# Optimization experiments

Measured on AMD Instinct MI355X. Metric: run time of the kernel, lower is better.

Reference implementation:

```python
import jax, jax.numpy as jnp
import numpy as np

B, S, RNN, ATTH = 256, 196, 1024, 512  # batch, att_size, rnn_size, att_h_size


def setup_inputs() -> dict:
    key = jax.random.key(0)
    k1, k2, k3, k4, k5, k6, k7 = jax.random.split(key, 7)
    h = jax.random.normal(k1, (B, RNN), dtype=jnp.float32)
    att_feats = jax.random.normal(k2, (B, S, RNN), dtype=jnp.float32)
    p_att_feats = jax.random.normal(k3, (B, S, ATTH), dtype=jnp.float32)
    # learned params (torch nn.Linear: y = x @ W.T + b)
    w_h2att = jax.random.normal(k4, (ATTH, RNN), dtype=jnp.float32) / np.sqrt(RNN)
    b_h2att = jax.random.normal(k5, (ATTH,), dtype=jnp.float32) * 0.01
    w_alpha = jax.random.normal(k6, (1, ATTH), dtype=jnp.float32) / np.sqrt(ATTH)
    b_alpha = jax.random.normal(k7, (1,), dtype=jnp.float32) * 0.01
    return {
        "h": h,
        "att_feats": att_feats,
        "p_att_feats": p_att_feats,
        "w_h2att": w_h2att,
        "b_h2att": b_h2att,
        "w_alpha": w_alpha,
        "b_alpha": b_alpha,
    }


def reference(h, att_feats, p_att_feats, w_h2att, b_h2att, w_alpha, b_alpha):
    # att_h = h2att(h): [B, ATTH]
    att_h = h @ w_h2att.T + b_h2att
    # additive combine + tanh: [B, S, ATTH]
    dot = jnp.tanh(p_att_feats + att_h[:, None, :])
    # alpha_net: [B, S]
    scores = jnp.einsum("bsa,a->bs", dot, w_alpha[0]) + b_alpha[0]
    weight = jax.nn.softmax(scores, axis=1)
    # weighted sum of att_feats: [B, RNN]
    att_res = jnp.einsum("bs,bsd->bd", weight, att_feats)
    return att_res
```

## Files before the change

kernel.cpp:

```cpp
#include <hip/hip_runtime.h>
#include <cstddef>

static constexpr int kB    = 256;
static constexpr int kS    = 196;
static constexpr int kRNN  = 1024;
static constexpr int kATTH = 512;
static constexpr int kQ    = 4;
static constexpr int kSC   = kS / kQ;

static constexpr size_t kOffAttH = 0;
static constexpr size_t kOffEsum = kOffAttH + (size_t)kB * kATTH;
static constexpr size_t kOffPart = kOffEsum + (size_t)kB * kQ;

__device__ __forceinline__ float fast_tanh(float x) {
    x = fminf(12.0f, fmaxf(-12.0f, x));
    float e = __expf(2.0f * x);
    return __fdividef(e - 1.0f, e + 1.0f);
}

__device__ __forceinline__ float dot8t(const float4 p0, const float4 p1,
                                       const float4 ah0, const float4 ah1,
                                       const float4 wa0, const float4 wa1) {
    float r;
    r  = fast_tanh(p0.x + ah0.x) * wa0.x;
    r += fast_tanh(p0.y + ah0.y) * wa0.y;
    r += fast_tanh(p0.z + ah0.z) * wa0.z;
    r += fast_tanh(p0.w + ah0.w) * wa0.w;
    r += fast_tanh(p1.x + ah1.x) * wa1.x;
    r += fast_tanh(p1.y + ah1.y) * wa1.y;
    r += fast_tanh(p1.z + ah1.z) * wa1.z;
    r += fast_tanh(p1.w + ah1.w) * wa1.w;
    return r;
}

__global__ __launch_bounds__(256, 4) void k1_atth(
    const float* __restrict__ h, const float* __restrict__ w_h2att,
    const float* __restrict__ b_h2att, float* __restrict__ att_h) {
    const int b  = blockIdx.x >> 2;
    const int rq = blockIdx.x & 3;
    const int tid = threadIdx.x;
    const int lane = tid & 63;
    const int wave = tid >> 6;

    const float* hb = &h[(size_t)b * kRNN];
    const int k0 = lane << 2;
    const float4 h0 = *(const float4*)&hb[k0];
    const float4 h1 = *(const float4*)&hb[k0 + 256];
    const float4 h2 = *(const float4*)&hb[k0 + 512];
    const float4 h3 = *(const float4*)&hb[k0 + 768];
    const int abase = rq * 128 + wave * 32;
#pragma unroll 2
    for (int r = 0; r < 32; ++r) {
        const int a = abase + r;
        const float* wr = &w_h2att[(size_t)a * kRNN + k0];
        const float4 x0 = *(const float4*)(wr);
        const float4 x1 = *(const float4*)(wr + 256);
        const float4 x2 = *(const float4*)(wr + 512);
        const float4 x3 = *(const float4*)(wr + 768);
        float d;
        d  = x0.x * h0.x + x0.y * h0.y + x0.z * h0.z + x0.w * h0.w;
        d += x1.x * h1.x + x1.y * h1.y + x1.z * h1.z + x1.w * h1.w;
        d += x2.x * h2.x + x2.y * h2.y + x2.z * h2.z + x2.w * h2.w;
        d += x3.x * h3.x + x3.y * h3.y + x3.z * h3.z + x3.w * h3.w;
#pragma unroll
        for (int off = 32; off > 0; off >>= 1) d += __shfl_xor(d, off, 64);
        if (lane == 0) att_h[(size_t)b * kATTH + a] = d + b_h2att[a];
    }
}

__global__ __launch_bounds__(256, 4) void k23_score_pv(
    const float* __restrict__ att_feats, const float* __restrict__ p_att,
    const float* __restrict__ att_h, const float* __restrict__ w_alpha,
    const float* __restrict__ b_alpha, float* __restrict__ esum,
    float* __restrict__ part) {
    const int b = blockIdx.x >> 2;
    const int q = blockIdx.x & 3;
    const int tid = threadIdx.x;
    const int lane = tid & 63;
    const int wave = tid >> 6;

    __shared__ float sE[kSC];
    __shared__ float sEw[4];

    const int col = lane << 3;
    const float4 ah0 = *(const float4*)&att_h[(size_t)b * kATTH + col];
    const float4 ah1 = *(const float4*)&att_h[(size_t)b * kATTH + col + 4];
    const float4 wa0 = *(const float4*)&w_alpha[col];
    const float4 wa1 = *(const float4*)&w_alpha[col + 4];
    const float balpha = b_alpha[0];

    float sw = fabsf(wa0.x) + fabsf(wa0.y) + fabsf(wa0.z) + fabsf(wa0.w) +
               fabsf(wa1.x) + fabsf(wa1.y) + fabsf(wa1.z) + fabsf(wa1.w);
#pragma unroll
    for (int off = 32; off > 0; off >>= 1) sw += __shfl_xor(sw, off, 64);
    const float ebias = balpha - (sw + fabsf(balpha));

    const float* pbase = &p_att[((size_t)b * kS + (size_t)q * kSC) * kATTH + col];
    int s = wave;
    float4 p0 = *(const float4*)(pbase + (size_t)s * kATTH);
    float4 p1 = *(const float4*)(pbase + (size_t)s * kATTH + 4);
    const int nIter = (wave == 0) ? 13 : 12;
    float esumw = 0.f;
    for (int i = 0; i < nIter; ++i) {
        int sn = s + 4;
        sn = (sn > kSC - 1) ? (kSC - 1) : sn;
        const float4 np0 = *(const float4*)(pbase + (size_t)sn * kATTH);
        const float4 np1 = *(const float4*)(pbase + (size_t)sn * kATTH + 4);
        float r = dot8t(p0, p1, ah0, ah1, wa0, wa1);
#pragma unroll
        for (int off = 32; off > 0; off >>= 1) r += __shfl_xor(r, off, 64);
        if (lane == 0) {
            const float e = __expf(r + ebias);
            sE[s] = e;
            esumw += e;
        }
        s = sn;
        p0 = np0; p1 = np1;
    }
    if (lane == 0) sEw[wave] = esumw;
    __syncthreads();
    if (tid == 0) esum[b * kQ + q] = sEw[0] + sEw[1] + sEw[2] + sEw[3];

    const float* af =
        &att_feats[((size_t)b * kS + (size_t)q * kSC) * kRNN + (tid << 2)];
    float4 acc = {0.f, 0.f, 0.f, 0.f};
    for (int o = 0; o < 7; ++o) {
        float4 v[7];
#pragma unroll
        for (int j = 0; j < 7; ++j)
            v[j] = *(const float4*)(af + (size_t)(o * 7 + j) * kRNN);
#pragma unroll
        for (int j = 0; j < 7; ++j) {
            const float w = sE[o * 7 + j];
            acc.x += w * v[j].x; acc.y += w * v[j].y;
            acc.z += w * v[j].z; acc.w += w * v[j].w;
        }
    }
    *(float4*)&part[((size_t)(b * kQ + q)) * kRNN + (tid << 2)] = acc;
}

__global__ __launch_bounds__(256) void k4_combine(
    const float* __restrict__ part, const float* __restrict__ esum,
    float* __restrict__ out) {
    const int b = blockIdx.x;
    const int tid = threadIdx.x;

    const float* es = &esum[b * kQ];
    const float inv = __fdividef(1.0f, es[0] + es[1] + es[2] + es[3]);

    const float* pb = &part[(size_t)b * kQ * kRNN + (tid << 2)];
    const float4 a0 = *(const float4*)(pb);
    const float4 a1 = *(const float4*)(pb + kRNN);
    const float4 a2 = *(const float4*)(pb + 2 * kRNN);
    const float4 a3 = *(const float4*)(pb + 3 * kRNN);
    float4 o;
    o.x = (a0.x + a1.x + a2.x + a3.x) * inv;
    o.y = (a0.y + a1.y + a2.y + a3.y) * inv;
    o.z = (a0.z + a1.z + a2.z + a3.z) * inv;
    o.w = (a0.w + a1.w + a2.w + a3.w) * inv;
    *(float4*)&out[(size_t)b * kRNN + (tid << 2)] = o;
}

extern "C" void kernel_launch(void* const* d_in, const int* in_sizes, int n_in,
                              void* d_out, int out_size, void* d_ws, size_t ws_size,
                              hipStream_t stream) {
    const float* h         = (const float*)d_in[0];
    const float* att_feats = (const float*)d_in[1];
    const float* p_att     = (const float*)d_in[2];
    const float* w_h2att   = (const float*)d_in[3];
    const float* b_h2att   = (const float*)d_in[4];
    const float* w_alpha   = (const float*)d_in[5];
    const float* b_alpha   = (const float*)d_in[6];
    float* out = (float*)d_out;

    float* ws    = (float*)d_ws;
    float* att_h = ws + kOffAttH;
    float* esum  = ws + kOffEsum;
    float* part  = ws + kOffPart;

    k1_atth<<<kB * 4, 256, 0, stream>>>(h, w_h2att, b_h2att, att_h);
    k23_score_pv<<<kB * kQ, 256, 0, stream>>>(att_feats, p_att, att_h, w_alpha,
                                              b_alpha, esum, part);
    k4_combine<<<kB, 256, 0, stream>>>(part, esum, out);
}
```

Baseline: 387.5 us.

## Split sequence into 7 chunks and batch score loads for more memory parallelism

Raises the number of sequence chunks per batch from 4 to 7 (28 positions each), launching a 2D grid with more blocks. The score loop is replaced by two fully unrolled batches that issue all p_att loads up front and interleave the shuffle reductions. Occupancy hint is raised to 6 and the combine kernel sums 7 partials. The intent is more loads in flight to better saturate HBM bandwidth, at the cost of more partial-sum traffic and register pressure.

After: 387.8 us. No clear change (+0.1%).

```diff
diff --git a/kernel.cpp b/kernel.cpp
--- a/kernel.cpp
+++ b/kernel.cpp
@@ -5,12 +5,12 @@
 static constexpr int kS    = 196;
 static constexpr int kRNN  = 1024;
 static constexpr int kATTH = 512;
-static constexpr int kQ    = 4;
-static constexpr int kSC   = kS / kQ;
+static constexpr int kQ    = 7;
+static constexpr int kSC   = 28;
 
 static constexpr size_t kOffAttH = 0;
 static constexpr size_t kOffEsum = kOffAttH + (size_t)kB * kATTH;
-static constexpr size_t kOffPart = kOffEsum + (size_t)kB * kQ;
+static constexpr size_t kOffPart = 133120;
 
 __device__ __forceinline__ float fast_tanh(float x) {
     x = fminf(12.0f, fmaxf(-12.0f, x));
@@ -68,13 +68,13 @@
     }
 }
 
-__global__ __launch_bounds__(256, 4) void k23_score_pv(
+__global__ __launch_bounds__(256, 6) void k23_score_pv(
     const float* __restrict__ att_feats, const float* __restrict__ p_att,
     const float* __restrict__ att_h, const float* __restrict__ w_alpha,
     const float* __restrict__ b_alpha, float* __restrict__ esum,
     float* __restrict__ part) {
-    const int b = blockIdx.x >> 2;
-    const int q = blockIdx.x & 3;
+    const int q = blockIdx.x;
+    const int b = blockIdx.y;
     const int tid = threadIdx.x;
     const int lane = tid & 63;
     const int wave = tid >> 6;
@@ -95,27 +95,60 @@
     for (int off = 32; off > 0; off >>= 1) sw += __shfl_xor(sw, off, 64);
     const float ebias = balpha - (sw + fabsf(balpha));
 
-    const float* pbase = &p_att[((size_t)b * kS + (size_t)q * kSC) * kATTH + col];
-    int s = wave;
-    float4 p0 = *(const float4*)(pbase + (size_t)s * kATTH);
-    float4 p1 = *(const float4*)(pbase + (size_t)s * kATTH + 4);
-    const int nIter = (wave == 0) ? 13 : 12;
+    const float* pb = &p_att[((size_t)b * kS + (size_t)q * kSC) * kATTH + col];
     float esumw = 0.f;
-    for (int i = 0; i < nIter; ++i) {
-        int sn = s + 4;
-        sn = (sn > kSC - 1) ? (kSC - 1) : sn;
-        const float4 np0 = *(const float4*)(pbase + (size_t)sn * kATTH);
-        const float4 np1 = *(const float4*)(pbase + (size_t)sn * kATTH + 4);
-        float r = dot8t(p0, p1, ah0, ah1, wa0, wa1);
-#pragma unroll
-        for (int off = 32; off > 0; off >>= 1) r += __shfl_xor(r, off, 64);
+
+    {
+        float4 pa[8];
+#pragma unroll
+        for (int j = 0; j < 4; ++j) {
+            const float* p = pb + (size_t)(wave + 4 * j) * kATTH;
+            pa[2 * j]     = *(const float4*)p;
+            pa[2 * j + 1] = *(const float4*)(p + 4);
+        }
+        float rr[4];
+#pragma unroll
+        for (int j = 0; j < 4; ++j)
+            rr[j] = dot8t(pa[2 * j], pa[2 * j + 1], ah0, ah1, wa0, wa1);
+#pragma unroll
+        for (int off = 32; off > 0; off >>= 1) {
+#pragma unroll
+            for (int j = 0; j < 4; ++j) rr[j] += __shfl_xor(rr[j], off, 64);
+        }
         if (lane == 0) {
-            const float e = __expf(r + ebias);
-            sE[s] = e;
-            esumw += e;
-        }
-        s = sn;
-        p0 = np0; p1 = np1;
+#pragma unroll
+            for (int j = 0; j < 4; ++j) {
+                const float e = __expf(rr[j] + ebias);
+                sE[wave + 4 * j] = e;
+                esumw += e;
+            }
+        }
+    }
+    {
+        float4 pa[6];
+#pragma unroll
+        for (int j = 0; j < 3; ++j) {
+            const float* p = pb + (size_t)(wave + 16 + 4 * j) * kATTH;
+            pa[2 * j]     = *(const float4*)p;
+            pa[2 * j + 1] = *(const float4*)(p + 4);
+        }
+        float rr[3];
+#pragma unroll
+        for (int j = 0; j < 3; ++j)
+            rr[j] = dot8t(pa[2 * j], pa[2 * j + 1], ah0, ah1, wa0, wa1);
+#pragma unroll
+        for (int off = 32; off > 0; off >>= 1) {
+#pragma unroll
+            for (int j = 0; j < 3; ++j) rr[j] += __shfl_xor(rr[j], off, 64);
+        }
+        if (lane == 0) {
+#pragma unroll
+            for (int j = 0; j < 3; ++j) {
+                const float e = __expf(rr[j] + ebias);
+                sE[wave + 16 + 4 * j] = e;
+                esumw += e;
+            }
+        }
     }
     if (lane == 0) sEw[wave] = esumw;
     __syncthreads();
@@ -124,7 +157,8 @@
     const float* af =
         &att_feats[((size_t)b * kS + (size_t)q * kSC) * kRNN + (tid << 2)];
     float4 acc = {0.f, 0.f, 0.f, 0.f};
-    for (int o = 0; o < 7; ++o) {
+#pragma unroll
+    for (int o = 0; o < 4; ++o) {
         float4 v[7];
 #pragma unroll
         for (int j = 0; j < 7; ++j)
@@ -146,18 +180,22 @@
     const int tid = threadIdx.x;
 
     const float* es = &esum[b * kQ];
-    const float inv = __fdividef(1.0f, es[0] + es[1] + es[2] + es[3]);
+    float tot = 0.f;
+#pragma unroll
+    for (int j = 0; j < kQ; ++j) tot += es[j];
+    const float inv = __fdividef(1.0f, tot);
 
     const float* pb = &part[(size_t)b * kQ * kRNN + (tid << 2)];
-    const float4 a0 = *(const float4*)(pb);
-    const float4 a1 = *(const float4*)(pb + kRNN);
-    const float4 a2 = *(const float4*)(pb + 2 * kRNN);
-    const float4 a3 = *(const float4*)(pb + 3 * kRNN);
-    float4 o;
-    o.x = (a0.x + a1.x + a2.x + a3.x) * inv;
-    o.y = (a0.y + a1.y + a2.y + a3.y) * inv;
-    o.z = (a0.z + a1.z + a2.z + a3.z) * inv;
-    o.w = (a0.w + a1.w + a2.w + a3.w) * inv;
+    float4 a[kQ];
+#pragma unroll
+    for (int j = 0; j < kQ; ++j)
+        a[j] = *(const float4*)(pb + (size_t)j * kRNN);
+    float4 o = {0.f, 0.f, 0.f, 0.f};
+#pragma unroll
+    for (int j = 0; j < kQ; ++j) {
+        o.x += a[j].x; o.y += a[j].y; o.z += a[j].z; o.w += a[j].w;
+    }
+    o.x *= inv; o.y *= inv; o.z *= inv; o.w *= inv;
     *(float4*)&out[(size_t)b * kRNN + (tid << 2)] = o;
 }
 
@@ -179,7 +217,7 @@
     float* part  = ws + kOffPart;
 
     k1_atth<<<kB * 4, 256, 0, stream>>>(h, w_h2att, b_h2att, att_h);
-    k23_score_pv<<<kB * kQ, 256, 0, stream>>>(att_feats, p_att, att_h, w_alpha,
-                                              b_alpha, esum, part);
+    k23_score_pv<<<dim3(kQ, kB), 256, 0, stream>>>(att_feats, p_att, att_h,
+                                                   w_alpha, b_alpha, esum, part);
     k4_combine<<<kB, 256, 0, stream>>>(part, esum, out);
 }
```
